# Kernel optimization log

Hardware: AMD Instinct MI355X
Metric: run time of the kernel (lower is better)

## Reference

```python
import jax, jax.numpy as jnp
import numpy as np

WEIGHT0 = 0.4
WEIGHT1 = 1.6
N = 16777216


def setup_inputs() -> dict:
    key = jax.random.key(0)
    k1, k2 = jax.random.split(key)
    inp = jax.random.uniform(k1, (N,), dtype=jnp.float32, minval=1e-6, maxval=1.0 - 1e-6)
    target = jax.random.randint(k2, (N,), 0, 2, dtype=jnp.int32)
    return {"input": inp, "target": target}


def reference(input, target):
    # per-element class-weighted log term: log(p)*w1 if target==1 else log(1-p)*w0
    is_pos = target == 1
    per_elem = jnp.where(is_pos,
                         jnp.log(input) * WEIGHT1,
                         jnp.log(1.0 - input) * WEIGHT0)
    n = input.shape[0]
    loss = -jnp.sum(per_elem) / n
    # accuracy: round(p) == target, fraction correct
    preds = jnp.round(input)
    acc = jnp.mean((preds == target.astype(input.dtype)).astype(jnp.float32))
    return (loss, acc)
```

## Files before the change

kernel.cpp:

```cpp
#include <hip/hip_runtime.h>
#include <hip/hip_bf16.h>

#define W0 0.4f
#define W1 1.6f


__global__ __launch_bounds__(256) void bce_reduce_kernel(
    const float4* __restrict__ in4,
    const int4* __restrict__ tg4,
    float* __restrict__ psum,
    unsigned int* __restrict__ pcnt)
{
    const int base = blockIdx.x * 1024 + threadIdx.x;

    float4 p0 = in4[base];
    float4 p1 = in4[base + 256];
    float4 p2 = in4[base + 512];
    float4 p3 = in4[base + 768];
    int4 t0 = tg4[base];
    int4 t1 = tg4[base + 256];
    int4 t2 = tg4[base + 512];
    int4 t3 = tg4[base + 768];

    float sum = 0.0f;
    unsigned int correct = 0;

#define ELEM(P, T)                                                   \
    {                                                                \
        bool pos = ((T) == 1);                                       \
        float x = pos ? (P) : (1.0f - (P));                          \
        float w = pos ? W1 : W0;                                     \
        sum = __builtin_fmaf(__logf(x), w, sum);                     \
        correct += (rintf(P) == (float)(T)) ? 1u : 0u;               \
    }

    ELEM(p0.x, t0.x) ELEM(p0.y, t0.y) ELEM(p0.z, t0.z) ELEM(p0.w, t0.w)
    ELEM(p1.x, t1.x) ELEM(p1.y, t1.y) ELEM(p1.z, t1.z) ELEM(p1.w, t1.w)
    ELEM(p2.x, t2.x) ELEM(p2.y, t2.y) ELEM(p2.z, t2.z) ELEM(p2.w, t2.w)
    ELEM(p3.x, t3.x) ELEM(p3.y, t3.y) ELEM(p3.z, t3.z) ELEM(p3.w, t3.w)
#undef ELEM

    #pragma unroll
    for (int off = 32; off > 0; off >>= 1) {
        sum     += __shfl_down(sum, off, 64);
        correct += __shfl_down(correct, off, 64);
    }

    __shared__ float s_sum[4];
    __shared__ unsigned int s_cnt[4];
    const int lane = threadIdx.x & 63;
    const int wave = threadIdx.x >> 6;
    if (lane == 0) { s_sum[wave] = sum; s_cnt[wave] = correct; }
    __syncthreads();
    if (threadIdx.x == 0) {
        float bs = s_sum[0] + s_sum[1] + s_sum[2] + s_sum[3];
        unsigned int bc = s_cnt[0] + s_cnt[1] + s_cnt[2] + s_cnt[3];
        psum[blockIdx.x] = bs;
        pcnt[blockIdx.x] = bc;
    }
}

__global__ __launch_bounds__(1024) void bce_finalize_kernel(
    const float* __restrict__ psum,
    const unsigned int* __restrict__ pcnt,
    float* __restrict__ out, int nblocks, int n)
{
    const int tid = threadIdx.x;
    double s = 0.0;
    unsigned long long c = 0;
    for (int k = tid; k < nblocks; k += 1024) {
        s += (double)psum[k];
        c += (unsigned long long)pcnt[k];
    }
    #pragma unroll
    for (int off = 32; off > 0; off >>= 1) {
        s += __shfl_down(s, off, 64);
        c += __shfl_down(c, off, 64);
    }
    __shared__ double sh_s[16];
    __shared__ unsigned long long sh_c[16];
    const int lane = tid & 63;
    const int wave = tid >> 6;
    if (lane == 0) { sh_s[wave] = s; sh_c[wave] = c; }
    __syncthreads();
    if (tid == 0) {
        double ts = 0.0;
        unsigned long long tc = 0;
        for (int w = 0; w < 16; ++w) { ts += sh_s[w]; tc += sh_c[w]; }
        double inv_n = 1.0 / (double)n;
        out[0] = (float)(-ts * inv_n);
        out[1] = (float)((double)tc * inv_n);
    }
}

extern "C" void kernel_launch(void* const* d_in, const int* in_sizes, int n_in,
                              void* d_out, int out_size, void* d_ws, size_t ws_size,
                              hipStream_t stream) {
    const float4* in4 = (const float4*)d_in[0];
    const int4*   tg4 = (const int4*)d_in[1];
    float* out = (float*)d_out;
    int n = in_sizes[0];
    int nblocks = n >> 12;

    float* psum = (float*)d_ws;
    unsigned int* pcnt = (unsigned int*)((char*)d_ws + (size_t)nblocks * sizeof(float));

    bce_reduce_kernel<<<nblocks, 256, 0, stream>>>(in4, tg4, psum, pcnt);
    bce_finalize_kernel<<<1, 1024, 0, stream>>>(psum, pcnt, out, nblocks, n);
}
```

Before: 144.3 us.

## Double the per-block work with a software-pipelined load loop and simpler accuracy test

Each block now handles 8192 elements instead of 4096, halving the grid and the partial-sum count. The loads go through an unrolled loop that prefetches the next float4/int4 pair while the current one is processed. The accuracy check uses p > 0.5 against the target flag instead of rintf and a compare. The target test becomes t != 0. The pipelined loop holds fewer loads in flight per thread than issuing all four up front, which may hurt memory-level parallelism, and the accuracy change differs from round-half-even only at exactly 0.5.

```diff
diff --git a/kernel.cpp b/kernel.cpp
--- a/kernel.cpp
+++ b/kernel.cpp
@@ -11,33 +11,36 @@
     float* __restrict__ psum,
     unsigned int* __restrict__ pcnt)
 {
-    const int base = blockIdx.x * 1024 + threadIdx.x;
+    const int idx = blockIdx.x * 2048 + threadIdx.x;
 
-    float4 p0 = in4[base];
-    float4 p1 = in4[base + 256];
-    float4 p2 = in4[base + 512];
-    float4 p3 = in4[base + 768];
-    int4 t0 = tg4[base];
-    int4 t1 = tg4[base + 256];
-    int4 t2 = tg4[base + 512];
-    int4 t3 = tg4[base + 768];
+    float4 p = in4[idx];
+    int4   t = tg4[idx];
 
     float sum = 0.0f;
     unsigned int correct = 0;
 
-#define ELEM(P, T)                                                   \
-    {                                                                \
-        bool pos = ((T) == 1);                                       \
-        float x = pos ? (P) : (1.0f - (P));                          \
-        float w = pos ? W1 : W0;                                     \
-        sum = __builtin_fmaf(__logf(x), w, sum);                     \
-        correct += (rintf(P) == (float)(T)) ? 1u : 0u;               \
+#define ELEM(P, T)                                                    \
+    {                                                                 \
+        bool pos = ((T) != 0);                                        \
+        float x = pos ? (P) : (1.0f - (P));                           \
+        float w = pos ? W1 : W0;                                      \
+        sum = __builtin_fmaf(__logf(x), w, sum);                      \
+        correct += (((P) > 0.5f) == pos) ? 1u : 0u;                   \
     }
 
-    ELEM(p0.x, t0.x) ELEM(p0.y, t0.y) ELEM(p0.z, t0.z) ELEM(p0.w, t0.w)
-    ELEM(p1.x, t1.x) ELEM(p1.y, t1.y) ELEM(p1.z, t1.z) ELEM(p1.w, t1.w)
-    ELEM(p2.x, t2.x) ELEM(p2.y, t2.y) ELEM(p2.z, t2.z) ELEM(p2.w, t2.w)
-    ELEM(p3.x, t3.x) ELEM(p3.y, t3.y) ELEM(p3.z, t3.z) ELEM(p3.w, t3.w)
+    #pragma unroll
+    for (int k = 0; k < 8; ++k) {
+        float4 pc = p;
+        int4   tc = t;
+        if (k < 7) {
+            p = in4[idx + (k + 1) * 256];
+            t = tg4[idx + (k + 1) * 256];
+        }
+        ELEM(pc.x, tc.x)
+        ELEM(pc.y, tc.y)
+        ELEM(pc.z, tc.z)
+        ELEM(pc.w, tc.w)
+    }
 #undef ELEM
 
     #pragma unroll
@@ -100,7 +103,7 @@
     const int4*   tg4 = (const int4*)d_in[1];
     float* out = (float*)d_out;
     int n = in_sizes[0];
-    int nblocks = n >> 12;
+    int nblocks = n >> 13;
 
     float* psum = (float*)d_ws;
     unsigned int* pcnt = (unsigned int*)((char*)d_ws + (size_t)nblocks * sizeof(float));
```

Result: no change. 145.4 us (+0.8%).

## Stage inputs through LDS with double-buffered async global_load_lds and larger per-block work

Applied to the files above, without the earlier changes.

Each block now handles 16384 elements in 8 tiles, prefetching the next tile straight into LDS with buffer-to-LDS async loads while computing the current one, using hand-placed waitcnt and barriers. This aims to keep more memory requests in flight and to cut the number of blocks and partial sums. The accuracy test is simplified to p>0.5 compared against target!=0. The cost is LDS round-trips, extra barriers and fewer blocks, which may reduce occupancy and latency hiding on a purely bandwidth-bound stream.

```diff
diff --git a/kernel.cpp b/kernel.cpp
--- a/kernel.cpp
+++ b/kernel.cpp
@@ -1,44 +1,80 @@
 #include <hip/hip_runtime.h>
-#include <hip/hip_bf16.h>
 
 #define W0 0.4f
 #define W1 1.6f
 
+#define TILE 2048
+#define TPB  16384
+#define NTILES (TPB / TILE)
 
-__global__ __launch_bounds__(256) void bce_reduce_kernel(
-    const float4* __restrict__ in4,
-    const int4* __restrict__ tg4,
+typedef __attribute__((address_space(3))) void lds_t;
+typedef const __attribute__((address_space(1))) void gbl_t;
+
+
+__global__ __launch_bounds__(256, 4) void bce_reduce_kernel(
+    const float* __restrict__ input,
+    const int* __restrict__ target,
     float* __restrict__ psum,
     unsigned int* __restrict__ pcnt)
 {
-    const int base = blockIdx.x * 1024 + threadIdx.x;
+    __shared__ float s_in[2][TILE];
+    __shared__ int   s_tg[2][TILE];
 
-    float4 p0 = in4[base];
-    float4 p1 = in4[base + 256];
-    float4 p2 = in4[base + 512];
-    float4 p3 = in4[base + 768];
-    int4 t0 = tg4[base];
-    int4 t1 = tg4[base + 256];
-    int4 t2 = tg4[base + 512];
-    int4 t3 = tg4[base + 768];
+    const int tid  = threadIdx.x;
+    const int wave = tid >> 6;
+    const int lane = tid & 63;
+    const long base = (long)blockIdx.x * TPB;
+
+#define STAGE(b, t)                                                            \
+    {                                                                          \
+        const long e0 = base + (long)(t) * TILE + wave * 512;                  \
+        const float* gi = input + e0 + lane * 4;                               \
+        const int*   gt = target + e0 + lane * 4;                              \
+        __builtin_amdgcn_global_load_lds((gbl_t*)(gi),                         \
+            (lds_t*)&s_in[b][wave * 512], 16, 0, 0);                           \
+        __builtin_amdgcn_global_load_lds((gbl_t*)(gi + 256),                   \
+            (lds_t*)&s_in[b][wave * 512 + 256], 16, 0, 0);                     \
+        __builtin_amdgcn_global_load_lds((gbl_t*)(gt),                         \
+            (lds_t*)&s_tg[b][wave * 512], 16, 0, 0);                           \
+        __builtin_amdgcn_global_load_lds((gbl_t*)(gt + 256),                   \
+            (lds_t*)&s_tg[b][wave * 512 + 256], 16, 0, 0);                     \
+    }
 
     float sum = 0.0f;
     unsigned int correct = 0;
 
-#define ELEM(P, T)                                                   \
-    {                                                                \
-        bool pos = ((T) == 1);                                       \
-        float x = pos ? (P) : (1.0f - (P));                          \
-        float w = pos ? W1 : W0;                                     \
-        sum = __builtin_fmaf(__logf(x), w, sum);                     \
-        correct += (rintf(P) == (float)(T)) ? 1u : 0u;               \
+#define ELEM(P, T)                                                             \
+    {                                                                          \
+        bool pos = ((T) != 0);                                                 \
+        float x = pos ? (P) : (1.0f - (P));                                    \
+        float w = pos ? W1 : W0;                                               \
+        sum = __builtin_fmaf(__logf(x), w, sum);                               \
+        correct += (((P) > 0.5f) == pos) ? 1u : 0u;                            \
     }
 
-    ELEM(p0.x, t0.x) ELEM(p0.y, t0.y) ELEM(p0.z, t0.z) ELEM(p0.w, t0.w)
-    ELEM(p1.x, t1.x) ELEM(p1.y, t1.y) ELEM(p1.z, t1.z) ELEM(p1.w, t1.w)
-    ELEM(p2.x, t2.x) ELEM(p2.y, t2.y) ELEM(p2.z, t2.z) ELEM(p2.w, t2.w)
-    ELEM(p3.x, t3.x) ELEM(p3.y, t3.y) ELEM(p3.z, t3.z) ELEM(p3.w, t3.w)
+    STAGE(0, 0);
+
+    #pragma unroll 1
+    for (int t = 0; t < NTILES; ++t) {
+        if (t + 1 < NTILES) {
+            STAGE((t + 1) & 1, t + 1);
+            asm volatile("s_waitcnt vmcnt(4)\n\ts_barrier" ::: "memory");
+        } else {
+            asm volatile("s_waitcnt vmcnt(0)\n\ts_barrier" ::: "memory");
+        }
+        const int b = t & 1;
+        float4 p0 = ((const float4*)s_in[b])[tid];
+        float4 p1 = ((const float4*)s_in[b])[tid + 256];
+        int4   t0 = ((const int4*)s_tg[b])[tid];
+        int4   t1 = ((const int4*)s_tg[b])[tid + 256];
+
+        ELEM(p0.x, t0.x) ELEM(p0.y, t0.y) ELEM(p0.z, t0.z) ELEM(p0.w, t0.w)
+        ELEM(p1.x, t1.x) ELEM(p1.y, t1.y) ELEM(p1.z, t1.z) ELEM(p1.w, t1.w)
+
+        asm volatile("s_barrier" ::: "memory");
+    }
 #undef ELEM
+#undef STAGE
 
     #pragma unroll
     for (int off = 32; off > 0; off >>= 1) {
@@ -48,11 +84,9 @@
 
     __shared__ float s_sum[4];
     __shared__ unsigned int s_cnt[4];
-    const int lane = threadIdx.x & 63;
-    const int wave = threadIdx.x >> 6;
     if (lane == 0) { s_sum[wave] = sum; s_cnt[wave] = correct; }
     __syncthreads();
-    if (threadIdx.x == 0) {
+    if (tid == 0) {
         float bs = s_sum[0] + s_sum[1] + s_sum[2] + s_sum[3];
         unsigned int bc = s_cnt[0] + s_cnt[1] + s_cnt[2] + s_cnt[3];
         psum[blockIdx.x] = bs;
@@ -96,15 +130,15 @@
 extern "C" void kernel_launch(void* const* d_in, const int* in_sizes, int n_in,
                               void* d_out, int out_size, void* d_ws, size_t ws_size,
                               hipStream_t stream) {
-    const float4* in4 = (const float4*)d_in[0];
-    const int4*   tg4 = (const int4*)d_in[1];
+    const float* input  = (const float*)d_in[0];
+    const int*   target = (const int*)d_in[1];
     float* out = (float*)d_out;
     int n = in_sizes[0];
-    int nblocks = n >> 12;
+    int nblocks = n / TPB;
 
     float* psum = (float*)d_ws;
     unsigned int* pcnt = (unsigned int*)((char*)d_ws + (size_t)nblocks * sizeof(float));
 
-    bce_reduce_kernel<<<nblocks, 256, 0, stream>>>(in4, tg4, psum, pcnt);
+    bce_reduce_kernel<<<nblocks, 256, 0, stream>>>(input, target, psum, pcnt);
     bce_finalize_kernel<<<1, 1024, 0, stream>>>(psum, pcnt, out, nblocks, n);
 }
```

Result: slower. 148.8 us (+3.2%).
